# Performance work log

Hardware: AMD Instinct MI355X
Metric: run time of the kernel (lower is better)

Reference implementation:

```python
import jax, jax.numpy as jnp
import numpy as np

N_NODES = 100000
N_EDGES = 1000000
F_IN = 256
HEADS = 2
C_OUT = 64
NEG_SLOPE = 0.2


def setup_inputs() -> dict:
    key = jax.random.key(0)
    k_x, k_e, k_ws, k_wd, k_a = jax.random.split(key, 5)
    x = jax.random.normal(k_x, (N_NODES, F_IN), dtype=jnp.float32)
    edge_index = jax.random.randint(k_e, (2, N_EDGES), 0, N_NODES, dtype=jnp.int64)
    # uniform init as in init_randoms('uniform'), scale is irrelevant for correctness
    W_src = jax.random.uniform(k_ws, (F_IN, HEADS * C_OUT), dtype=jnp.float32, minval=-0.1, maxval=0.1)
    W_dst = jax.random.uniform(k_wd, (F_IN, HEADS * C_OUT), dtype=jnp.float32, minval=-0.1, maxval=0.1)
    att = jax.random.uniform(k_a, (HEADS, C_OUT), dtype=jnp.float32, minval=-0.1, maxval=0.1)
    bias = jnp.zeros((HEADS * C_OUT,), dtype=jnp.float32)
    return {"x": x, "edge_index": edge_index, "W_src": W_src, "W_dst": W_dst, "att": att, "bias": bias}


def reference(x, edge_index, W_src, W_dst, att, bias):
    # GATv2 conv (MyGATConv), concat=True, add_self_loops=False, dropout=0
    N = x.shape[0]
    H, C = att.shape
    x_src = (x @ W_src).reshape(N, H, C)  # Theta_s x  [N,H,C]
    x_dst = (x @ W_dst).reshape(N, H, C)  # Theta_d x  [N,H,C]
    src = edge_index[0]  # j (source)
    dst = edge_index[1]  # i (target) -> segment index

    xj = x_src[src]                                   # [E,H,C]
    e = jax.nn.leaky_relu(xj + x_dst[dst], NEG_SLOPE)  # [E,H,C]
    logits = jnp.einsum('ehc,hc->eh', e, att)          # [E,H]

    # segment softmax over destination neighborhoods
    seg_max = jax.ops.segment_max(logits, dst, num_segments=N)  # [N,H]
    seg_max = jnp.where(jnp.isfinite(seg_max), seg_max, 0.0)
    ex = jnp.exp(logits - seg_max[dst])                # [E,H]
    denom = jax.ops.segment_sum(ex, dst, num_segments=N)  # [N,H]
    alpha = ex / (denom[dst] + 1e-16)                  # [E,H]

    # scatter-add aggregation of alpha * Theta_s x_j
    out = jax.ops.segment_sum(alpha[:, :, None] * xj, dst, num_segments=N)  # [N,H,C]
    return out.reshape(N, H * C) + bias
```

## Files before the change

kernel.cpp:

```cpp
#include <hip/hip_runtime.h>

#define F_IN 256
#define HC   128

typedef __attribute__((ext_vector_type(8))) short bf16x8;
typedef __attribute__((ext_vector_type(4))) float f32x4;

__device__ __forceinline__ unsigned short f2b(float f) {
    unsigned int u = __float_as_uint(f);
    return (unsigned short)((u + 0x7FFFu + ((u >> 16) & 1u)) >> 16);
}

__device__ __forceinline__ unsigned int f2b_pk(float lo, float hi) {
    unsigned int ul = __float_as_uint(lo);
    unsigned int uh = __float_as_uint(hi);
    ul = ul + 0x7FFFu + ((ul >> 16) & 1u);
    uh = uh + 0x7FFFu + ((uh >> 16) & 1u);
    return __builtin_amdgcn_perm(uh, ul, 0x07060302);
}

#define DPP_ADD(x, ctrl) \
    x += __int_as_float(__builtin_amdgcn_update_dpp(0, __float_as_int(x), ctrl, 0xF, 0xF, true))

__device__ __forceinline__ float row_sum16(float x) {
    DPP_ADD(x, 0xB1);
    DPP_ADD(x, 0x4E);
    DPP_ADD(x, 0x141);
    DPP_ADD(x, 0x140);
    return x;
}

#define CONV_BLOCKS 2048
__global__ __launch_bounds__(256) void k_prep(const float* __restrict__ x,
                                              unsigned short* __restrict__ xb, long nx,
                                              const float* __restrict__ Ws,
                                              const float* __restrict__ Wd,
                                              unsigned short* __restrict__ PB) {
    int b = blockIdx.x;
    if (b < CONV_BLOCKS) {
        long i = ((long)b * 256 + threadIdx.x) * 8;
        long stride = (long)CONV_BLOCKS * 256 * 8;
        for (; i < nx; i += stride) {
            float4 a = *(const float4*)(x + i);
            float4 c = *(const float4*)(x + i + 4);
            uint4 o;
            o.x = f2b_pk(a.x, a.y); o.y = f2b_pk(a.z, a.w);
            o.z = f2b_pk(c.x, c.y); o.w = f2b_pk(c.z, c.w);
            *(uint4*)(xb + i) = o;
        }
    } else {
        int tid = (b - CONV_BLOCKS) * 256 + threadIdx.x;
        int nt  = tid >> 9;
        int rem = tid & 511;
        int t   = rem >> 6;
        int l   = rem & 63;
        int n     = nt * 16 + (l & 15);
        int kbase = 32 * t + (l >> 4) * 8;
        union { bf16x8 v; unsigned short u[8]; } o;
#pragma unroll
        for (int j = 0; j < 8; ++j) {
            int k = kbase + j;
            float w = (n < HC) ? Ws[k * HC + n] : Wd[k * HC + (n - HC)];
            o.u[j] = f2b(w);
        }
        *(bf16x8*)(PB + (size_t)tid * 8) = o.v;
    }
}

#define LIST_BLOCKS 1024
__global__ __launch_bounds__(256) void k_gemm_list(const unsigned short* __restrict__ xb,
                                                   const unsigned short* __restrict__ PB,
                                                   unsigned short* __restrict__ xsrc_pk,
                                                   unsigned short* __restrict__ xdst_pk, int N,
                                                   const int* __restrict__ src,
                                                   const int* __restrict__ dst, int E,
                                                   int* __restrict__ head4,
                                                   uint2* __restrict__ rec) {
    if (blockIdx.x < LIST_BLOCKS) {
        int i = blockIdx.x * 256 + threadIdx.x;
        int stride = LIST_BLOCKS * 256;
        for (; i < E; i += stride) {
            int d = dst[i];
            int s = src[i];
            int old = atomicExch(&head4[(size_t)d * 4 + (i & 3)], i);
            rec[i] = make_uint2((unsigned int)old, (unsigned int)s);
        }
        return;
    }

    const int wave = threadIdx.x >> 6;
    const int lane = threadIdx.x & 63;
    const int m = lane & 15;
    const int q = lane >> 4;
    const long row0 = (long)(blockIdx.x - LIST_BLOCKS) * 64;

    f32x4 acc[4][4];
#pragma unroll
    for (int a = 0; a < 4; ++a)
#pragma unroll
        for (int b = 0; b < 4; ++b) acc[a][b] = (f32x4){0.f, 0.f, 0.f, 0.f};

    long rl[4];
#pragma unroll
    for (int mt = 0; mt < 4; ++mt) {
        long r = row0 + mt * 16 + m;
        rl[mt] = (r < N) ? r : (long)(N - 1);
    }

#pragma unroll
    for (int t = 0; t < 8; ++t) {
        const int k0 = t * 32 + q * 8;
        bf16x8 af[4];
#pragma unroll
        for (int mt = 0; mt < 4; ++mt)
            af[mt] = *(const bf16x8*)(xb + rl[mt] * F_IN + k0);
#pragma unroll
        for (int g = 0; g < 4; ++g) {
            const int nt = wave * 4 + g;
            bf16x8 bf = *(const bf16x8*)(PB + ((size_t)(nt * 8 + t) * 64 + lane) * 8);
#pragma unroll
            for (int mt = 0; mt < 4; ++mt)
                acc[mt][g] = __builtin_amdgcn_mfma_f32_16x16x32_bf16(af[mt], bf, acc[mt][g], 0, 0, 0);
        }
    }

#pragma unroll
    for (int mt = 0; mt < 4; ++mt) {
#pragma unroll
        for (int g = 0; g < 4; ++g) {
            const int nt = wave * 4 + g;
            const int n  = nt * 16 + m;
#pragma unroll
            for (int r = 0; r < 4; ++r) {
                long row = row0 + mt * 16 + q * 4 + r;
                if (row >= N) continue;
                unsigned short v = f2b(acc[mt][g][r]);
                if (n < HC) {
                    int h = n >> 6, c = n & 63;
                    xsrc_pk[row * HC + c * 2 + h] = v;
                } else {
                    int h = (n - HC) >> 6, c = (n - HC) & 63;
                    xdst_pk[row * HC + c * 2 + h] = v;
                }
            }
        }
    }
}

__global__ __launch_bounds__(256) void k_agg(const unsigned int* __restrict__ xsrc_u,
                                             const unsigned int* __restrict__ xdst_u,
                                             const int* __restrict__ head4,
                                             const uint2* __restrict__ rec,
                                             const float* __restrict__ att,
                                             const float* __restrict__ bias,
                                             float* __restrict__ out, int N) {
    int wid  = threadIdx.x >> 6;
    int lane = threadIdx.x & 63;
    int node = blockIdx.x * 4 + wid;
    if (node >= N) return;
    int g = lane >> 4;
    int s = lane & 15;

    uint4 D = *(const uint4*)(xdst_u + (size_t)node * 64 + s * 4);
    float xd0[4], xd1[4];
    {
        unsigned int du[4] = {D.x, D.y, D.z, D.w};
#pragma unroll
        for (int k = 0; k < 4; ++k) {
            xd0[k] = __uint_as_float(du[k] << 16);
            xd1[k] = __uint_as_float(du[k] & 0xFFFF0000u);
        }
    }
    float4 A0 = *(const float4*)(att + s * 4);
    float4 A1 = *(const float4*)(att + 64 + s * 4);
    float c10[4] = {0.6f * A0.x, 0.6f * A0.y, 0.6f * A0.z, 0.6f * A0.w};
    float c20[4] = {0.4f * A0.x, 0.4f * A0.y, 0.4f * A0.z, 0.4f * A0.w};
    float c11[4] = {0.6f * A1.x, 0.6f * A1.y, 0.6f * A1.z, 0.6f * A1.w};
    float c21[4] = {0.4f * A1.x, 0.4f * A1.y, 0.4f * A1.z, 0.4f * A1.w};

    float l0 = 0.f, l1 = 0.f;
    float o0[4] = {0.f, 0.f, 0.f, 0.f}, o1[4] = {0.f, 0.f, 0.f, 0.f};

    int e = head4[(size_t)node * 4 + g];
    uint2 r;
    if (e >= 0) r = rec[e];
    while (__any(e >= 0)) {
        if (e >= 0) {
            int j = (int)r.y;
            uint4 U = *(const uint4*)(xsrc_u + (size_t)j * 64 + s * 4);
            int en = (int)r.x;
            if (en >= 0) r = rec[en];
            unsigned int cu[4] = {U.x, U.y, U.z, U.w};
            float xj0[4], xj1[4];
            float s0 = 0.f, s1 = 0.f;
#pragma unroll
            for (int k = 0; k < 4; ++k) {
                xj0[k] = __uint_as_float(cu[k] << 16);
                xj1[k] = __uint_as_float(cu[k] & 0xFFFF0000u);
                float e0 = xj0[k] + xd0[k];
                float e1 = xj1[k] + xd1[k];
                s0 = fmaf(c10[k], e0, s0); s0 = fmaf(c20[k], fabsf(e0), s0);
                s1 = fmaf(c11[k], e1, s1); s1 = fmaf(c21[k], fabsf(e1), s1);
            }
            s0 = row_sum16(s0);
            s1 = row_sum16(s1);
            float w0 = __expf(s0);
            float w1 = __expf(s1);
            l0 += w0; l1 += w1;
#pragma unroll
            for (int k = 0; k < 4; ++k) {
                o0[k] = fmaf(w0, xj0[k], o0[k]);
                o1[k] = fmaf(w1, xj1[k], o1[k]);
            }
            e = en;
        }
    }

#define XRED(v) { v += __shfl_xor(v, 16, 64); v += __shfl_xor(v, 32, 64); }
    XRED(l0); XRED(l1);
#pragma unroll
    for (int k = 0; k < 4; ++k) { XRED(o0[k]); XRED(o1[k]); }
#undef XRED

    if (g == 0) {
        float inv0 = __builtin_amdgcn_rcpf(l0 + 1e-16f);
        float inv1 = __builtin_amdgcn_rcpf(l1 + 1e-16f);
        float4 B0 = *(const float4*)(bias + s * 4);
        float4 B1 = *(const float4*)(bias + 64 + s * 4);
        float4 R0 = {o0[0] * inv0 + B0.x, o0[1] * inv0 + B0.y,
                     o0[2] * inv0 + B0.z, o0[3] * inv0 + B0.w};
        float4 R1 = {o1[0] * inv1 + B1.x, o1[1] * inv1 + B1.y,
                     o1[2] * inv1 + B1.z, o1[3] * inv1 + B1.w};
        *(float4*)(out + (size_t)node * HC + s * 4) = R0;
        *(float4*)(out + (size_t)node * HC + 64 + s * 4) = R1;
    }
}

extern "C" void kernel_launch(void* const* d_in, const int* in_sizes, int n_in,
                              void* d_out, int out_size, void* d_ws, size_t ws_size,
                              hipStream_t stream) {
    const float* x    = (const float*)d_in[0];
    const int*   ei   = (const int*)d_in[1];
    const float* Ws   = (const float*)d_in[2];
    const float* Wd   = (const float*)d_in[3];
    const float* att  = (const float*)d_in[4];
    const float* bias = (const float*)d_in[5];
    float* out = (float*)d_out;

    const int N = in_sizes[0] / F_IN;
    const int E = in_sizes[1] / 2;
    const int* src = ei;
    const int* dst = ei + E;

    char* ws = (char*)d_ws;
    size_t off = 0;
    auto alloc = [&](size_t bytes) -> char* {
        off = (off + 255) & ~(size_t)255;
        char* p = ws + off;
        off += bytes;
        return p;
    };
    unsigned short* xb      = (unsigned short*)alloc((size_t)N * F_IN * sizeof(unsigned short));
    unsigned short* xsrc_pk = (unsigned short*)alloc((size_t)N * HC * sizeof(unsigned short));
    unsigned short* xdst_pk = (unsigned short*)alloc((size_t)N * HC * sizeof(unsigned short));
    unsigned short* PB = (unsigned short*)alloc(256 * 256 * sizeof(unsigned short));
    int*   head4 = (int*)alloc((size_t)N * 4 * sizeof(int));
    uint2* rec   = (uint2*)alloc((size_t)E * sizeof(uint2));

    hipMemsetAsync(head4, 0xFF, (size_t)N * 4 * sizeof(int), stream);

    k_prep<<<CONV_BLOCKS + 32, 256, 0, stream>>>(x, xb, (long)N * F_IN, Ws, Wd, PB);
    k_gemm_list<<<LIST_BLOCKS + (N + 63) / 64, 256, 0, stream>>>(
        xb, PB, xsrc_pk, xdst_pk, N, src, dst, E, head4, rec);
    k_agg<<<(N + 3) / 4, 256, 0, stream>>>((const unsigned int*)xsrc_pk,
                                           (const unsigned int*)xdst_pk,
                                           head4, rec, att, bias, out, N);
}
```

Baseline: 326.6 us.

## Fuse x bf16 conversion into GEMM and permute weight columns for packed stores

The separate pass that converted x to a bf16 buffer is removed; the GEMM now reads fp32 x directly and converts to bf16 in registers. The weight packing permutes output columns so each lane owns four consecutive packed (c,h) outputs, which turns the scattered 2-byte epilogue stores into one 8-byte store per row. Row tile is halved to 32 rows per block and the edge-list block count is doubled. This removes a full write and re-read of the bf16 copy of x, but the GEMM now loads twice as many bytes of x per tile.

```diff
diff --git a/kernel.cpp b/kernel.cpp
--- a/kernel.cpp
+++ b/kernel.cpp
@@ -30,45 +30,37 @@
     return x;
 }
 
-#define CONV_BLOCKS 2048
-__global__ __launch_bounds__(256) void k_prep(const float* __restrict__ x,
-                                              unsigned short* __restrict__ xb, long nx,
-                                              const float* __restrict__ Ws,
+__global__ __launch_bounds__(256) void k_prep(const float* __restrict__ Ws,
                                               const float* __restrict__ Wd,
                                               unsigned short* __restrict__ PB) {
-    int b = blockIdx.x;
-    if (b < CONV_BLOCKS) {
-        long i = ((long)b * 256 + threadIdx.x) * 8;
-        long stride = (long)CONV_BLOCKS * 256 * 8;
-        for (; i < nx; i += stride) {
-            float4 a = *(const float4*)(x + i);
-            float4 c = *(const float4*)(x + i + 4);
-            uint4 o;
-            o.x = f2b_pk(a.x, a.y); o.y = f2b_pk(a.z, a.w);
-            o.z = f2b_pk(c.x, c.y); o.w = f2b_pk(c.z, c.w);
-            *(uint4*)(xb + i) = o;
-        }
+    int tid = blockIdx.x * 256 + threadIdx.x;
+    int nt  = tid >> 9;
+    int rem = tid & 511;
+    int t   = rem >> 6;
+    int l   = rem & 63;
+    int m   = l & 15;
+    int w   = nt >> 2;
+    int g   = nt & 3;
+    int pos = w * 64 + m * 4 + g;
+    int kbase = 32 * t + (l >> 4) * 8;
+
+    const float* W;
+    int n;
+    if (pos < 128) {
+        W = Ws; n = (pos & 1) * 64 + (pos >> 1);
     } else {
-        int tid = (b - CONV_BLOCKS) * 256 + threadIdx.x;
-        int nt  = tid >> 9;
-        int rem = tid & 511;
-        int t   = rem >> 6;
-        int l   = rem & 63;
-        int n     = nt * 16 + (l & 15);
-        int kbase = 32 * t + (l >> 4) * 8;
-        union { bf16x8 v; unsigned short u[8]; } o;
-#pragma unroll
-        for (int j = 0; j < 8; ++j) {
-            int k = kbase + j;
-            float w = (n < HC) ? Ws[k * HC + n] : Wd[k * HC + (n - HC)];
-            o.u[j] = f2b(w);
-        }
-        *(bf16x8*)(PB + (size_t)tid * 8) = o.v;
-    }
-}
-
-#define LIST_BLOCKS 1024
-__global__ __launch_bounds__(256) void k_gemm_list(const unsigned short* __restrict__ xb,
+        int p2 = pos - 128;
+        W = Wd; n = (p2 & 1) * 64 + (p2 >> 1);
+    }
+    union { bf16x8 v; unsigned short u[8]; } o;
+#pragma unroll
+    for (int j = 0; j < 8; ++j)
+        o.u[j] = f2b(W[(kbase + j) * HC + n]);
+    *(bf16x8*)(PB + (size_t)tid * 8) = o.v;
+}
+
+#define LIST_BLOCKS 2048
+__global__ __launch_bounds__(256) void k_gemm_list(const float* __restrict__ x,
                                                    const unsigned short* __restrict__ PB,
                                                    unsigned short* __restrict__ xsrc_pk,
                                                    unsigned short* __restrict__ xdst_pk, int N,
@@ -92,17 +84,17 @@
     const int lane = threadIdx.x & 63;
     const int m = lane & 15;
     const int q = lane >> 4;
-    const long row0 = (long)(blockIdx.x - LIST_BLOCKS) * 64;
-
-    f32x4 acc[4][4];
-#pragma unroll
-    for (int a = 0; a < 4; ++a)
+    const long row0 = (long)(blockIdx.x - LIST_BLOCKS) * 32;
+
+    f32x4 acc[2][4];
+#pragma unroll
+    for (int a = 0; a < 2; ++a)
 #pragma unroll
         for (int b = 0; b < 4; ++b) acc[a][b] = (f32x4){0.f, 0.f, 0.f, 0.f};
 
-    long rl[4];
-#pragma unroll
-    for (int mt = 0; mt < 4; ++mt) {
+    long rl[2];
+#pragma unroll
+    for (int mt = 0; mt < 2; ++mt) {
         long r = row0 + mt * 16 + m;
         rl[mt] = (r < N) ? r : (long)(N - 1);
     }
@@ -110,39 +102,40 @@
 #pragma unroll
     for (int t = 0; t < 8; ++t) {
         const int k0 = t * 32 + q * 8;
-        bf16x8 af[4];
-#pragma unroll
-        for (int mt = 0; mt < 4; ++mt)
-            af[mt] = *(const bf16x8*)(xb + rl[mt] * F_IN + k0);
+        bf16x8 af[2];
+#pragma unroll
+        for (int mt = 0; mt < 2; ++mt) {
+            const float* p = x + rl[mt] * F_IN + k0;
+            float4 a = *(const float4*)p;
+            float4 c = *(const float4*)(p + 4);
+            union { bf16x8 v; unsigned int u[4]; } cv;
+            cv.u[0] = f2b_pk(a.x, a.y);
+            cv.u[1] = f2b_pk(a.z, a.w);
+            cv.u[2] = f2b_pk(c.x, c.y);
+            cv.u[3] = f2b_pk(c.z, c.w);
+            af[mt] = cv.v;
+        }
 #pragma unroll
         for (int g = 0; g < 4; ++g) {
             const int nt = wave * 4 + g;
             bf16x8 bf = *(const bf16x8*)(PB + ((size_t)(nt * 8 + t) * 64 + lane) * 8);
-#pragma unroll
-            for (int mt = 0; mt < 4; ++mt)
-                acc[mt][g] = __builtin_amdgcn_mfma_f32_16x16x32_bf16(af[mt], bf, acc[mt][g], 0, 0, 0);
-        }
-    }
-
-#pragma unroll
-    for (int mt = 0; mt < 4; ++mt) {
-#pragma unroll
-        for (int g = 0; g < 4; ++g) {
-            const int nt = wave * 4 + g;
-            const int n  = nt * 16 + m;
-#pragma unroll
-            for (int r = 0; r < 4; ++r) {
-                long row = row0 + mt * 16 + q * 4 + r;
-                if (row >= N) continue;
-                unsigned short v = f2b(acc[mt][g][r]);
-                if (n < HC) {
-                    int h = n >> 6, c = n & 63;
-                    xsrc_pk[row * HC + c * 2 + h] = v;
-                } else {
-                    int h = (n - HC) >> 6, c = (n - HC) & 63;
-                    xdst_pk[row * HC + c * 2 + h] = v;
-                }
-            }
+            acc[0][g] = __builtin_amdgcn_mfma_f32_16x16x32_bf16(af[0], bf, acc[0][g], 0, 0, 0);
+            acc[1][g] = __builtin_amdgcn_mfma_f32_16x16x32_bf16(af[1], bf, acc[1][g], 0, 0, 0);
+        }
+    }
+
+    unsigned short* dstArr = (wave < 2) ? xsrc_pk : xdst_pk;
+    const int colOff = ((wave & 1) * 64) + m * 4;
+#pragma unroll
+    for (int mt = 0; mt < 2; ++mt) {
+#pragma unroll
+        for (int r = 0; r < 4; ++r) {
+            long row = row0 + mt * 16 + q * 4 + r;
+            if (row >= N) continue;
+            uint2 v;
+            v.x = f2b_pk(acc[mt][0][r], acc[mt][1][r]);
+            v.y = f2b_pk(acc[mt][2][r], acc[mt][3][r]);
+            *(uint2*)(dstArr + row * HC + colOff) = v;
         }
     }
 }
@@ -260,7 +253,6 @@
         off += bytes;
         return p;
     };
-    unsigned short* xb      = (unsigned short*)alloc((size_t)N * F_IN * sizeof(unsigned short));
     unsigned short* xsrc_pk = (unsigned short*)alloc((size_t)N * HC * sizeof(unsigned short));
     unsigned short* xdst_pk = (unsigned short*)alloc((size_t)N * HC * sizeof(unsigned short));
     unsigned short* PB = (unsigned short*)alloc(256 * 256 * sizeof(unsigned short));
@@ -269,9 +261,9 @@
 
     hipMemsetAsync(head4, 0xFF, (size_t)N * 4 * sizeof(int), stream);
 
-    k_prep<<<CONV_BLOCKS + 32, 256, 0, stream>>>(x, xb, (long)N * F_IN, Ws, Wd, PB);
-    k_gemm_list<<<LIST_BLOCKS + (N + 63) / 64, 256, 0, stream>>>(
-        xb, PB, xsrc_pk, xdst_pk, N, src, dst, E, head4, rec);
+    k_prep<<<32, 256, 0, stream>>>(Ws, Wd, PB);
+    k_gemm_list<<<LIST_BLOCKS + (N + 31) / 32, 256, 0, stream>>>(
+        x, PB, xsrc_pk, xdst_pk, N, src, dst, E, head4, rec);
     k_agg<<<(N + 3) / 4, 256, 0, stream>>>((const unsigned int*)xsrc_pk,
                                            (const unsigned int*)xdst_pk,
                                            head4, rec, att, bias, out, N);
```

After: 323.0 us. Within noise of the previous version (-1.1%).
